# Kernel tuning notes

Measured on AMD Instinct MI355X. Metric: run time of the kernel, lower is better.

## Reference

```python
import jax, jax.numpy as jnp
import numpy as np

N = 50000
E = 800000
IN_DIM = 64
OUT_DIM = 64


def setup_inputs() -> dict:
    key = jax.random.key(0)
    k_x, k_e, k_ws, k_wn, k_bs, k_bn = jax.random.split(key, 6)
    x = jax.random.normal(k_x, (N, IN_DIM), dtype=jnp.float32)
    edge_index = jax.random.randint(k_e, (2, E), 0, N, dtype=jnp.int64)
    # nn.Linear default init: U(-1/sqrt(fan_in), 1/sqrt(fan_in))
    bound = 1.0 / np.sqrt(IN_DIM)
    W_self = jax.random.uniform(k_ws, (OUT_DIM, IN_DIM), minval=-bound, maxval=bound, dtype=jnp.float32)
    b_self = jax.random.uniform(k_bs, (OUT_DIM,), minval=-bound, maxval=bound, dtype=jnp.float32)
    W_neigh = jax.random.uniform(k_wn, (OUT_DIM, IN_DIM), minval=-bound, maxval=bound, dtype=jnp.float32)
    b_neigh = jax.random.uniform(k_bn, (OUT_DIM,), minval=-bound, maxval=bound, dtype=jnp.float32)
    return {"x": x, "edge_index": edge_index, "W_self": W_self, "b_self": b_self,
            "W_neigh": W_neigh, "b_neigh": b_neigh}


def reference(x, edge_index, W_self, b_self, W_neigh, b_neigh):
    src, dst = edge_index[0], edge_index[1]
    # scatter-add of gathered neighbor features into src rows: agg[src] += x[dst]
    agg = jax.ops.segment_sum(x[dst], src, num_segments=N)            # [N, in_dim]
    deg = jax.ops.segment_sum(jnp.ones((E,), dtype=x.dtype), src, num_segments=N)
    deg = jnp.clip(deg, 1.0, None)[:, None]                            # [N, 1]
    agg = agg / deg
    out = x @ W_self.T + b_self + agg @ W_neigh.T + b_neigh            # [N, out_dim]
    return jax.nn.relu(out)
```

## Files before the change

kernel.cpp:

```cpp
#include <hip/hip_runtime.h>


#define N_NODES 50000
#define N_EDGES 800000
#define DIM 64
#define NBUCKET 196
#define BUCKET_SLOTS 4608
#define CELL 64
#define CHUNK_E 4096
#define NBIN 196
#define NCONV 782

typedef __attribute__((ext_vector_type(8))) short bf16x8;
typedef __attribute__((ext_vector_type(4))) float f32x4;

__device__ __forceinline__ unsigned short f2bf(float f) {
    unsigned int b = __float_as_uint(f);
    b = (b + 0x7FFFu + ((b >> 16) & 1u)) >> 16;
    return (unsigned short)b;
}
__device__ __forceinline__ float bf2f(unsigned short u) {
    return __uint_as_float(((unsigned int)u) << 16);
}

__global__ __launch_bounds__(1024) void build_conv(
    const float* __restrict__ x,
    const int* __restrict__ src,
    const int* __restrict__ dst,
    unsigned short* __restrict__ xb,
    const float* __restrict__ Ws,
    const float* __restrict__ Wn,
    unsigned short* __restrict__ Wsb,
    unsigned short* __restrict__ Wnb,
    int* __restrict__ bh,
    unsigned int* __restrict__ staging)
{
    __shared__ int hist[NBUCKET];
    __shared__ int lcur[NBUCKET];
    const int g = blockIdx.x;
    const int t = threadIdx.x;

    if (g < NBIN) {
        if (t < NBUCKET) { hist[t] = 0; lcur[t] = 0; }
        __syncthreads();
        const int base = g * CHUNK_E;
        int b_[4];
        unsigned int enc_[4];
#pragma unroll
        for (int i = 0; i < 4; ++i) {
            int e = base + i * 1024 + t;
            bool valid = (e < N_EDGES);
            int s = valid ? src[e] : 0;
            int d = valid ? dst[e] : 0;
            b_[i] = valid ? (s >> 8) : -1;
            enc_[i] = (((unsigned)s & 255u) << 16) | (unsigned)d;
            if (valid) atomicAdd(&hist[s >> 8], 1);
        }
        __syncthreads();
        if (t < NBUCKET) bh[g * NBUCKET + t] = hist[t];
#pragma unroll
        for (int i = 0; i < 4; ++i) {
            int b = b_[i];
            if (b >= 0) {
                int p = atomicAdd(&lcur[b], 1);
                if (p < CELL)
                    staging[((size_t)g * NBUCKET + b) * CELL + p] = enc_[i];
            }
        }
    } else if (g < NBIN + NCONV) {
        int i = (g - NBIN) * 1024 + t;
        if (i < N_NODES * DIM / 4) {
            float4 v = reinterpret_cast<const float4*>(x)[i];
            ushort4 u;
            u.x = f2bf(v.x); u.y = f2bf(v.y); u.z = f2bf(v.z); u.w = f2bf(v.w);
            reinterpret_cast<ushort4*>(xb)[i] = u;
        }
    } else {
        for (int i = t; i < DIM * DIM; i += 1024) {
            Wsb[i] = f2bf(Ws[i]);
            Wnb[i] = f2bf(Wn[i]);
        }
    }
}

__global__ __launch_bounds__(1024) void pass2_csr(
    const int* __restrict__ bh,
    const unsigned int* __restrict__ staging,
    unsigned short* __restrict__ col16,
    unsigned int* __restrict__ offsdeg)
{
    __shared__ int runbase[NBUCKET + 1];
    __shared__ unsigned int compact[BUCKET_SLOTS];
    __shared__ int hist[256];
    __shared__ int lcur[256];
    __shared__ int wsum[4];
    __shared__ int hcol[256];
    const int t = threadIdx.x;
    const int b = blockIdx.x;
    const int lane = t & 63;
    const int w4 = t >> 6;

    if (t < 256) {
        int h = 0;
        if (t < NBUCKET) {
            h = bh[t * NBUCKET + b];
            if (h > CELL) h = CELL;
        }
        hcol[t] = h;
        hist[t] = 0;
    }
    __syncthreads();

    if (t < 256) {
        int val = hcol[t];
        int v = val;
#pragma unroll
        for (int off = 1; off < 64; off <<= 1) {
            int u = __shfl_up(v, off);
            if (lane >= off) v += u;
        }
        if (lane == 63) wsum[w4] = v;
        __syncthreads();
        int woff = 0;
        for (int k = 0; k < w4; ++k) woff += wsum[k];
        if (t <= NBUCKET) runbase[t] = woff + (v - val);
    } else {
        __syncthreads();
    }
    __syncthreads();
    const int nb = runbase[NBUCKET];

    for (int i = t; i < nb; i += 1024) {
        int lo = 0, hi = NBUCKET;
        while (hi - lo > 1) {
            int mid = (lo + hi) >> 1;
            if (runbase[mid] <= i) lo = mid; else hi = mid;
        }
        compact[i] = staging[((size_t)lo * NBUCKET + b) * CELL + (i - runbase[lo])];
    }
    __syncthreads();

    for (int i = t; i < nb; i += 1024)
        atomicAdd(&hist[compact[i] >> 16], 1);
    __syncthreads();

    if (t < 256) {
        int h = hist[t];
        int v = h;
#pragma unroll
        for (int off = 1; off < 64; off <<= 1) {
            int u = __shfl_up(v, off);
            if (lane >= off) v += u;
        }
        if (lane == 63) wsum[w4] = v;
        __syncthreads();
        int woff = 0;
        for (int k = 0; k < w4; ++k) woff += wsum[k];
        int excl = woff + (v - h);
        lcur[t] = excl;
        offsdeg[b * 256 + t] = ((unsigned)h << 24)
                             | (unsigned)(b * BUCKET_SLOTS + excl);
    } else {
        __syncthreads();
    }
    __syncthreads();

    for (int i = t; i < nb; i += 1024) {
        unsigned int enc = compact[i];
        int nl = enc >> 16;
        int p = atomicAdd(&lcur[nl], 1);
        col16[(size_t)b * BUCKET_SLOTS + p] = (unsigned short)(enc & 0xFFFFu);
    }
}

__device__ __forceinline__ float batch8(const unsigned short* __restrict__ xb,
                                        int cv, int k, int lane)
{
    int d0 = __builtin_amdgcn_readlane(cv, k + 0);
    int d1 = __builtin_amdgcn_readlane(cv, k + 1);
    int d2 = __builtin_amdgcn_readlane(cv, k + 2);
    int d3 = __builtin_amdgcn_readlane(cv, k + 3);
    int d4 = __builtin_amdgcn_readlane(cv, k + 4);
    int d5 = __builtin_amdgcn_readlane(cv, k + 5);
    int d6 = __builtin_amdgcn_readlane(cv, k + 6);
    int d7 = __builtin_amdgcn_readlane(cv, k + 7);
    float t0 = bf2f(xb[d0 * DIM + lane]) + bf2f(xb[d1 * DIM + lane]);
    float t1 = bf2f(xb[d2 * DIM + lane]) + bf2f(xb[d3 * DIM + lane]);
    float t2 = bf2f(xb[d4 * DIM + lane]) + bf2f(xb[d5 * DIM + lane]);
    float t3 = bf2f(xb[d6 * DIM + lane]) + bf2f(xb[d7 * DIM + lane]);
    return (t0 + t1) + (t2 + t3);
}

__device__ __forceinline__ float finish8(const unsigned short* __restrict__ xb,
                                         int cv, int k, int m, int lane)
{
    float s = 0.0f;
    for (; k + 8 <= m; k += 8) s += batch8(xb, cv, k, lane);
    for (; k < m; ++k) {
        int d = __builtin_amdgcn_readlane(cv, k);
        s += bf2f(xb[d * DIM + lane]);
    }
    return s;
}

__device__ __noinline__ float gather_long(const unsigned short* __restrict__ xb,
                                          const unsigned short* __restrict__ col16,
                                          int beg, int deg, int lane)
{
    float s = 0.0f;
    for (int base = 0; base < deg; base += 64) {
        int m = deg - base; if (m > 64) m = 64;
        int li = lane < m ? lane : m - 1;
        int cv = (int)col16[beg + base + li];
        s += finish8(xb, cv, 0, m, lane);
    }
    return s;
}

__global__ __launch_bounds__(256) void sage_fused(
    const unsigned short* __restrict__ xb,
    const unsigned short* __restrict__ col16,
    const unsigned int* __restrict__ offsdeg,
    const unsigned short* __restrict__ Wsb,
    const unsigned short* __restrict__ Wnb,
    const float* __restrict__ bs,
    const float* __restrict__ bn,
    float* __restrict__ out)
{
    __shared__ unsigned short as[16][72];
    const int t = threadIdx.x;
    const int lane = t & 63;
    const int w = t >> 6;
    const int nbase = blockIdx.x * 16;

    int beg0, beg1, beg2, beg3, deg0, deg1, deg2, deg3;
    {
        unsigned a = __builtin_amdgcn_readfirstlane(offsdeg[nbase + w * 4 + 0]);
        unsigned b = __builtin_amdgcn_readfirstlane(offsdeg[nbase + w * 4 + 1]);
        unsigned c = __builtin_amdgcn_readfirstlane(offsdeg[nbase + w * 4 + 2]);
        unsigned d = __builtin_amdgcn_readfirstlane(offsdeg[nbase + w * 4 + 3]);
        beg0 = (int)(a & 0xFFFFFFu); deg0 = (int)(a >> 24);
        beg1 = (int)(b & 0xFFFFFFu); deg1 = (int)(b >> 24);
        beg2 = (int)(c & 0xFFFFFFu); deg2 = (int)(c >> 24);
        beg3 = (int)(d & 0xFFFFFFu); deg3 = (int)(d >> 24);
    }
    int li0 = lane < deg0 ? lane : (deg0 > 0 ? deg0 - 1 : 0);
    int li1 = lane < deg1 ? lane : (deg1 > 0 ? deg1 - 1 : 0);
    int li2 = lane < deg2 ? lane : (deg2 > 0 ? deg2 - 1 : 0);
    int li3 = lane < deg3 ? lane : (deg3 > 0 ? deg3 - 1 : 0);
    int cv0 = (int)col16[beg0 + li0];
    int cv1 = (int)col16[beg1 + li1];
    int cv2 = (int)col16[beg2 + li2];
    int cv3 = (int)col16[beg3 + li3];

    float s0, s1, s2, s3;
    if ((deg0 | deg1 | deg2 | deg3) <= 64) {
        int m01 = deg0 < deg1 ? deg0 : deg1;
        int m23 = deg2 < deg3 ? deg2 : deg3;
        int mc = (m01 < m23 ? m01 : m23) & ~7;
        s0 = 0.f; s1 = 0.f; s2 = 0.f; s3 = 0.f;
        int k = 0;
        for (; k < mc; k += 8) {
            s0 += batch8(xb, cv0, k, lane);
            s1 += batch8(xb, cv1, k, lane);
            s2 += batch8(xb, cv2, k, lane);
            s3 += batch8(xb, cv3, k, lane);
        }
        s0 += finish8(xb, cv0, k, deg0, lane);
        s1 += finish8(xb, cv1, k, deg1, lane);
        s2 += finish8(xb, cv2, k, deg2, lane);
        s3 += finish8(xb, cv3, k, deg3, lane);
    } else {
        s0 = gather_long(xb, col16, beg0, deg0, lane);
        s1 = gather_long(xb, col16, beg1, deg1, lane);
        s2 = gather_long(xb, col16, beg2, deg2, lane);
        s3 = gather_long(xb, col16, beg3, deg3, lane);
    }
    as[w * 4 + 0][lane] = f2bf(s0 * (1.0f / (float)(deg0 > 0 ? deg0 : 1)));
    as[w * 4 + 1][lane] = f2bf(s1 * (1.0f / (float)(deg1 > 0 ? deg1 : 1)));
    as[w * 4 + 2][lane] = f2bf(s2 * (1.0f / (float)(deg2 > 0 ? deg2 : 1)));
    as[w * 4 + 3][lane] = f2bf(s3 * (1.0f / (float)(deg3 > 0 ? deg3 : 1)));
    __syncthreads();

    const int obase = w * 16;
    const int r  = lane & 15;
    const int kg = lane >> 4;

    const short* __restrict__ xr = (const short*)xb  + (size_t)(nbase + r) * DIM + kg * 8;
    const short* __restrict__ ws = (const short*)Wsb + (size_t)(obase + r) * DIM + kg * 8;
    const short* __restrict__ wn = (const short*)Wnb + (size_t)(obase + r) * DIM + kg * 8;
    const short* __restrict__ ar = (const short*)&as[r][kg * 8];

    f32x4 acc = {0.f, 0.f, 0.f, 0.f};
    {
        bf16x8 a0 = *reinterpret_cast<const bf16x8*>(xr);
        bf16x8 b0 = *reinterpret_cast<const bf16x8*>(ws);
        acc = __builtin_amdgcn_mfma_f32_16x16x32_bf16(a0, b0, acc, 0, 0, 0);
        bf16x8 a1 = *reinterpret_cast<const bf16x8*>(xr + 32);
        bf16x8 b1 = *reinterpret_cast<const bf16x8*>(ws + 32);
        acc = __builtin_amdgcn_mfma_f32_16x16x32_bf16(a1, b1, acc, 0, 0, 0);
        bf16x8 a2 = *reinterpret_cast<const bf16x8*>(ar);
        bf16x8 b2 = *reinterpret_cast<const bf16x8*>(wn);
        acc = __builtin_amdgcn_mfma_f32_16x16x32_bf16(a2, b2, acc, 0, 0, 0);
        bf16x8 a3 = *reinterpret_cast<const bf16x8*>(ar + 32);
        bf16x8 b3 = *reinterpret_cast<const bf16x8*>(wn + 32);
        acc = __builtin_amdgcn_mfma_f32_16x16x32_bf16(a3, b3, acc, 0, 0, 0);
    }

    const float bias = bs[obase + r] + bn[obase + r];
#pragma unroll
    for (int j = 0; j < 4; ++j) {
        int node = nbase + kg * 4 + j;
        out[(size_t)node * DIM + obase + r] = fmaxf(acc[j] + bias, 0.0f);
    }
}

extern "C" void kernel_launch(void* const* d_in, const int* in_sizes, int n_in,
                              void* d_out, int out_size, void* d_ws, size_t ws_size,
                              hipStream_t stream)
{
    const float* x      = (const float*)d_in[0];
    const int*   ei     = (const int*)d_in[1];
    const float* Wself  = (const float*)d_in[2];
    const float* bself  = (const float*)d_in[3];
    const float* Wneigh = (const float*)d_in[4];
    const float* bneigh = (const float*)d_in[5];
    float* out = (float*)d_out;

    int* bh               = (int*)d_ws;
    unsigned int* staging = (unsigned int*)(bh + NBIN * NBUCKET);
    unsigned short* col16 = (unsigned short*)(staging + (size_t)NBIN * NBUCKET * CELL);
    unsigned int* offsdeg = (unsigned int*)(col16 + (size_t)NBUCKET * BUCKET_SLOTS);
    unsigned short* xb    = (unsigned short*)(offsdeg + NBUCKET * 256);
    unsigned short* Wsb   = xb + (size_t)N_NODES * DIM;
    unsigned short* Wnb   = Wsb + DIM * DIM;

    const int* src = ei;
    const int* dst = ei + N_EDGES;

    build_conv<<<NBIN + NCONV + 1, 1024, 0, stream>>>(
        x, src, dst, xb, Wself, Wneigh, Wsb, Wnb, bh, staging);

    pass2_csr<<<NBUCKET, 1024, 0, stream>>>(bh, staging, col16, offsdeg);

    sage_fused<<<N_NODES / 16, 256, 0, stream>>>(xb, col16, offsdeg,
                                                 Wsb, Wnb, bself, bneigh, out);
}
```

Baseline: 63.15 us.

## Gather two nodes per wavefront with half-wave 32-bit loads

Restructures the neighbor aggregation so each half of a 64-lane wavefront handles a different node, with each lane loading two bf16 features as one 32-bit word instead of one 16-bit value per lane. Two nodes are processed per pass with predicated zeroing for lanes past the degree, replacing the separate short/long degree paths with a single 32-neighbor chunk loop. This is meant to halve the number of gather instructions and widen each memory access. In exchange, both halves run to the larger of the paired degrees, adding masked loads, and readlane selection adds some overhead.

```diff
diff --git a/kernel.cpp b/kernel.cpp
--- a/kernel.cpp
+++ b/kernel.cpp
@@ -18,9 +18,6 @@
     unsigned int b = __float_as_uint(f);
     b = (b + 0x7FFFu + ((b >> 16) & 1u)) >> 16;
     return (unsigned short)b;
-}
-__device__ __forceinline__ float bf2f(unsigned short u) {
-    return __uint_as_float(((unsigned int)u) << 16);
 }
 
 __global__ __launch_bounds__(1024) void build_conv(
@@ -173,50 +170,6 @@
     }
 }
 
-__device__ __forceinline__ float batch8(const unsigned short* __restrict__ xb,
-                                        int cv, int k, int lane)
-{
-    int d0 = __builtin_amdgcn_readlane(cv, k + 0);
-    int d1 = __builtin_amdgcn_readlane(cv, k + 1);
-    int d2 = __builtin_amdgcn_readlane(cv, k + 2);
-    int d3 = __builtin_amdgcn_readlane(cv, k + 3);
-    int d4 = __builtin_amdgcn_readlane(cv, k + 4);
-    int d5 = __builtin_amdgcn_readlane(cv, k + 5);
-    int d6 = __builtin_amdgcn_readlane(cv, k + 6);
-    int d7 = __builtin_amdgcn_readlane(cv, k + 7);
-    float t0 = bf2f(xb[d0 * DIM + lane]) + bf2f(xb[d1 * DIM + lane]);
-    float t1 = bf2f(xb[d2 * DIM + lane]) + bf2f(xb[d3 * DIM + lane]);
-    float t2 = bf2f(xb[d4 * DIM + lane]) + bf2f(xb[d5 * DIM + lane]);
-    float t3 = bf2f(xb[d6 * DIM + lane]) + bf2f(xb[d7 * DIM + lane]);
-    return (t0 + t1) + (t2 + t3);
-}
-
-__device__ __forceinline__ float finish8(const unsigned short* __restrict__ xb,
-                                         int cv, int k, int m, int lane)
-{
-    float s = 0.0f;
-    for (; k + 8 <= m; k += 8) s += batch8(xb, cv, k, lane);
-    for (; k < m; ++k) {
-        int d = __builtin_amdgcn_readlane(cv, k);
-        s += bf2f(xb[d * DIM + lane]);
-    }
-    return s;
-}
-
-__device__ __noinline__ float gather_long(const unsigned short* __restrict__ xb,
-                                          const unsigned short* __restrict__ col16,
-                                          int beg, int deg, int lane)
-{
-    float s = 0.0f;
-    for (int base = 0; base < deg; base += 64) {
-        int m = deg - base; if (m > 64) m = 64;
-        int li = lane < m ? lane : m - 1;
-        int cv = (int)col16[beg + base + li];
-        s += finish8(xb, cv, 0, m, lane);
-    }
-    return s;
-}
-
 __global__ __launch_bounds__(256) void sage_fused(
     const unsigned short* __restrict__ xb,
     const unsigned short* __restrict__ col16,
@@ -231,6 +184,8 @@
     const int t = threadIdx.x;
     const int lane = t & 63;
     const int w = t >> 6;
+    const int half = lane >> 5;
+    const int hl = lane & 31;
     const int nbase = blockIdx.x * 16;
 
     int beg0, beg1, beg2, beg3, deg0, deg1, deg2, deg3;
@@ -244,42 +199,59 @@
         beg2 = (int)(c & 0xFFFFFFu); deg2 = (int)(c >> 24);
         beg3 = (int)(d & 0xFFFFFFu); deg3 = (int)(d >> 24);
     }
-    int li0 = lane < deg0 ? lane : (deg0 > 0 ? deg0 - 1 : 0);
-    int li1 = lane < deg1 ? lane : (deg1 > 0 ? deg1 - 1 : 0);
-    int li2 = lane < deg2 ? lane : (deg2 > 0 ? deg2 - 1 : 0);
-    int li3 = lane < deg3 ? lane : (deg3 > 0 ? deg3 - 1 : 0);
-    int cv0 = (int)col16[beg0 + li0];
-    int cv1 = (int)col16[beg1 + li1];
-    int cv2 = (int)col16[beg2 + li2];
-    int cv3 = (int)col16[beg3 + li3];
-
-    float s0, s1, s2, s3;
-    if ((deg0 | deg1 | deg2 | deg3) <= 64) {
-        int m01 = deg0 < deg1 ? deg0 : deg1;
-        int m23 = deg2 < deg3 ? deg2 : deg3;
-        int mc = (m01 < m23 ? m01 : m23) & ~7;
-        s0 = 0.f; s1 = 0.f; s2 = 0.f; s3 = 0.f;
-        int k = 0;
-        for (; k < mc; k += 8) {
-            s0 += batch8(xb, cv0, k, lane);
-            s1 += batch8(xb, cv1, k, lane);
-            s2 += batch8(xb, cv2, k, lane);
-            s3 += batch8(xb, cv3, k, lane);
-        }
-        s0 += finish8(xb, cv0, k, deg0, lane);
-        s1 += finish8(xb, cv1, k, deg1, lane);
-        s2 += finish8(xb, cv2, k, deg2, lane);
-        s3 += finish8(xb, cv3, k, deg3, lane);
-    } else {
-        s0 = gather_long(xb, col16, beg0, deg0, lane);
-        s1 = gather_long(xb, col16, beg1, deg1, lane);
-        s2 = gather_long(xb, col16, beg2, deg2, lane);
-        s3 = gather_long(xb, col16, beg3, deg3, lane);
-    }
-    as[w * 4 + 0][lane] = f2bf(s0 * (1.0f / (float)(deg0 > 0 ? deg0 : 1)));
-    as[w * 4 + 1][lane] = f2bf(s1 * (1.0f / (float)(deg1 > 0 ? deg1 : 1)));
-    as[w * 4 + 2][lane] = f2bf(s2 * (1.0f / (float)(deg2 > 0 ? deg2 : 1)));
-    as[w * 4 + 3][lane] = f2bf(s3 * (1.0f / (float)(deg3 > 0 ? deg3 : 1)));
+    const int mselA = half ? deg1 : deg0;
+    const int bghA  = half ? beg1 : beg0;
+    const int mselB = half ? deg3 : deg2;
+    const int bghB  = half ? beg3 : beg2;
+    const int mxA = deg0 > deg1 ? deg0 : deg1;
+    const int mxB = deg2 > deg3 ? deg2 : deg3;
+    const int mx  = mxA > mxB ? mxA : mxB;
+
+    float sA0 = 0.f, sA1 = 0.f, sB0 = 0.f, sB1 = 0.f;
+
+#define STEP(cv, msel, base, jj, s0, s1)                                    \
+    {                                                                       \
+        int dA_ = __builtin_amdgcn_readlane(cv, jj);                        \
+        int dB_ = __builtin_amdgcn_readlane(cv, 32 + (jj));                 \
+        int d_  = half ? dB_ : dA_;                                         \
+        unsigned u_ = *reinterpret_cast<const unsigned*>(xb + d_ * DIM + hl * 2); \
+        u_ = ((base) + (jj) < (msel)) ? u_ : 0u;                            \
+        s0 += __uint_as_float(u_ << 16);                                    \
+        s1 += __uint_as_float(u_ & 0xFFFF0000u);                            \
+    }
+
+    for (int base = 0; base < mx; base += 32) {
+        int ia = base + hl;
+        int liA = (ia < mselA) ? ia : (mselA > 0 ? mselA - 1 : 0);
+        int liB = (ia < mselB) ? ia : (mselB > 0 ? mselB - 1 : 0);
+        int cvA = (int)col16[bghA + liA];
+        int cvB = (int)col16[bghB + liB];
+        int capA = mxA - base; capA = capA < 0 ? 0 : (capA > 32 ? 32 : capA);
+        int capB = mxB - base; capB = capB < 0 ? 0 : (capB > 32 ? 32 : capB);
+        int capm = capA > capB ? capA : capB;
+        for (int j = 0; j < capm; j += 8) {
+            if (j < capA) {
+#pragma unroll
+                for (int i = 0; i < 8; ++i) STEP(cvA, mselA, base, j + i, sA0, sA1)
+            }
+            if (j < capB) {
+#pragma unroll
+                for (int i = 0; i < 8; ++i) STEP(cvB, mselB, base, j + i, sB0, sB1)
+            }
+        }
+    }
+#undef STEP
+
+    {
+        float invA = 1.0f / (float)(mselA > 0 ? mselA : 1);
+        unsigned pkA = (unsigned)f2bf(sA0 * invA)
+                     | ((unsigned)f2bf(sA1 * invA) << 16);
+        *reinterpret_cast<unsigned*>(&as[w * 4 + half][hl * 2]) = pkA;
+        float invB = 1.0f / (float)(mselB > 0 ? mselB : 1);
+        unsigned pkB = (unsigned)f2bf(sB0 * invB)
+                     | ((unsigned)f2bf(sB1 * invB) << 16);
+        *reinterpret_cast<unsigned*>(&as[w * 4 + 2 + half][hl * 2]) = pkB;
+    }
     __syncthreads();
 
     const int obase = w * 16;
```

New measurement: 53.53 us. 15.2% less time.
